# Kernel tuning notes

Hardware: AMD Instinct MI355X
Metric: run time of the kernel (lower is better)

Reference implementation:

```python
import jax, jax.numpy as jnp
import numpy as np

D_MODEL = 256
NHEAD = 8
HEAD_DIM = D_MODEL // NHEAD
CLIP = 10.0


def setup_inputs() -> dict:
    key = jax.random.key(0)
    k1, k2, k3, k4 = jax.random.split(key, 4)
    B, N = 4, 256
    nodes = jax.random.normal(k1, (B, N, D_MODEL), dtype=jnp.float32)
    edges = jax.random.normal(k2, (B, N, N, D_MODEL), dtype=jnp.float32)
    # torch nn.Linear default init: U(-1/sqrt(in), 1/sqrt(in))
    bound = 1.0 / np.sqrt(D_MODEL)
    W = jax.random.uniform(k3, (D_MODEL, D_MODEL), minval=-bound, maxval=bound, dtype=jnp.float32)
    b = jax.random.uniform(k4, (D_MODEL,), minval=-bound, maxval=bound, dtype=jnp.float32)
    return {"nodes": nodes, "edges": edges, "W": W, "b": b}


def reference(nodes, edges, W, b):
    B, N, _ = nodes.shape
    H, Dh = NHEAD, HEAD_DIM

    def proj(x):  # torch Linear: x @ W.T + b
        return x @ W.T + b

    # Node projections: the module applies the SAME linear to q, k, v
    node_p = proj(nodes).reshape(B, N, H, Dh)
    nq, nk, nv = node_p, node_p, node_p
    # Edge projections (same linear for q and k)
    edge_p = proj(edges).reshape(B, N, N, H, Dh)
    eq, ek = edge_p, edge_p

    query = eq + nq[:, :, None, :, :]   # (B,N,N,H,Dh)
    key = ek + nk[:, None, :, :, :]     # (B,N,N,H,Dh)
    scores = jnp.einsum('bijhd,bijhd->bhij', query, key) / np.sqrt(Dh).astype(np.float32)
    scores = CLIP * jnp.tanh(scores)
    attn = jax.nn.softmax(scores, axis=-1)  # (B,H,N,N)
    # output = attn @ values (values transposed to (B,H,N,Dh))
    out = jnp.einsum('bhij,bjhd->bihd', attn, nv).reshape(B, N, D_MODEL)
    out = proj(out)
    return (out, attn)
```

## Files before the change

### kernel.cpp

```cpp
#include <hip/hip_runtime.h>
#include <hip/hip_bf16.h>
#include <math.h>

typedef short short8 __attribute__((ext_vector_type(8)));
typedef float f32x4 __attribute__((ext_vector_type(4)));

__device__ __forceinline__ unsigned short f2bf(float x) {
    unsigned u = __float_as_uint(x);
    u += 0x7FFF + ((u >> 16) & 1);
    return (unsigned short)(u >> 16);
}
__device__ __forceinline__ float bf2f(unsigned short h) {
    return __uint_as_float(((unsigned)h) << 16);
}

__device__ __forceinline__ void cvt2(float f0, float f1,
                                     unsigned short& h0, unsigned short& h1,
                                     unsigned short& l0, unsigned short& l1) {
    __hip_bfloat162 h = __float22bfloat162_rn(float2{f0, f1});
    unsigned hu = *(unsigned*)&h;
    h0 = (unsigned short)(hu & 0xFFFFu);
    h1 = (unsigned short)(hu >> 16);
    float r0 = f0 - __uint_as_float((hu & 0xFFFFu) << 16);
    float r1 = f1 - __uint_as_float(hu & 0xFFFF0000u);
    __hip_bfloat162 lo = __float22bfloat162_rn(float2{r0, r1});
    unsigned lu = *(unsigned*)&lo;
    l0 = (unsigned short)(lu & 0xFFFFu);
    l1 = (unsigned short)(lu >> 16);
}

__device__ __forceinline__ float tanh10(float y) {
    float e = __expf(2.f * y);
    return 10.f * (e - 1.f) / (e + 1.f);
}

#define GLDS16(gp, lp)                                                        \
    __builtin_amdgcn_global_load_lds(                                         \
        (const __attribute__((address_space(1))) void*)(gp),                  \
        (__attribute__((address_space(3))) void*)(lp), 16, 0, 0)

__global__ __launch_bounds__(256) void k_prep(const float* __restrict__ W,
                                              float* __restrict__ Wt,
                                              unsigned short* __restrict__ Whi,
                                              unsigned short* __restrict__ Wlo) {
    int d = blockIdx.x, k = threadIdx.x;
    float w = W[d * 256 + k];
    Wt[k * 256 + d] = w;
    unsigned short hi = f2bf(w);
    Whi[d * 256 + k] = hi;
    Wlo[d * 256 + k] = f2bf(w - bf2f(hi));
}

__global__ __launch_bounds__(256) void k_node_proj(const float* __restrict__ nodes,
                                                   const float* __restrict__ Wt,
                                                   const float* __restrict__ bias,
                                                   float* __restrict__ np_) {
    int row = blockIdx.x;
    int d = threadIdx.x;
    __shared__ float xl[256];
    xl[d] = nodes[row * 256 + d];
    __syncthreads();
    float a[8] = {0.f, 0.f, 0.f, 0.f, 0.f, 0.f, 0.f, 0.f};
#pragma unroll 4
    for (int k = 0; k < 256; k += 8) {
#pragma unroll
        for (int q = 0; q < 8; ++q)
            a[q] = fmaf(xl[k + q], Wt[(k + q) * 256 + d], a[q]);
    }
    np_[row * 256 + d] =
        bias[d] + ((a[0] + a[1]) + (a[2] + a[3])) + ((a[4] + a[5]) + (a[6] + a[7]));
}

__global__ __launch_bounds__(256) void k_edge_mfma(const float* __restrict__ edges,
                                                   const unsigned short* __restrict__ Whi,
                                                   const unsigned short* __restrict__ Wlo,
                                                   const float* __restrict__ bias,
                                                   const float* __restrict__ np_,
                                                   float* __restrict__ attn) {
    __shared__ unsigned short Eh[128 * 32], El[128 * 32];
    __shared__ unsigned short Wh[128 * 32], Wl[128 * 32];
    __shared__ float npi[128];
    __shared__ float sc[4][128];

    const int t = threadIdx.x;
    const int w = t >> 6, l = t & 63;
    const int tile = blockIdx.x >> 1;
    const int half = blockIdx.x & 1;
    const int m0 = tile * 128;
    const int bb = m0 >> 16;
    const int ii = (m0 >> 8) & 255;
    const int j0 = m0 & 255;
    const int n0 = half * 128;

    if (t < 32)
        ((float4*)npi)[t] = ((const float4*)(np_ + (size_t)(bb * 256 + ii) * 256 + n0))[t];

    f32x4 acc[4][4];
#pragma unroll
    for (int mt = 0; mt < 4; ++mt)
#pragma unroll
        for (int nt = 0; nt < 4; ++nt) acc[mt][nt] = (f32x4){0.f, 0.f, 0.f, 0.f};

    const int er = t >> 1, ehk = t & 1;
    const float* esrc = edges + (size_t)(m0 + er) * 256 + ehk * 16;

    const int wrow = (l >> 2), wq = l & 3;

    const int col = l & 15, g = l >> 4;
    const int wm = (w & 1) * 64, wn = (w >> 1) * 64;

    float4 ecur[4], enext[4];
#pragma unroll
    for (int q = 0; q < 4; ++q) ecur[q] = *(const float4*)(esrc + q * 4);

    for (int kc = 0; kc < 8; ++kc) {
#pragma unroll
        for (int s = 0; s < 2; ++s) {
            int base = w * 32 + s * 16;
            const unsigned short* gh =
                Whi + (size_t)(n0 + base + wrow) * 256 + kc * 32 + wq * 8;
            const unsigned short* gl =
                Wlo + (size_t)(n0 + base + wrow) * 256 + kc * 32 + wq * 8;
            GLDS16(gh, Wh + base * 32);
            GLDS16(gl, Wl + base * 32);
        }
        {
            unsigned short hi[16], lo[16];
#pragma unroll
            for (int q = 0; q < 4; ++q) {
                cvt2(ecur[q].x, ecur[q].y, hi[q * 4 + 0], hi[q * 4 + 1],
                     lo[q * 4 + 0], lo[q * 4 + 1]);
                cvt2(ecur[q].z, ecur[q].w, hi[q * 4 + 2], hi[q * 4 + 3],
                     lo[q * 4 + 2], lo[q * 4 + 3]);
            }
            *(short8*)(Eh + er * 32 + ehk * 16)     = *(short8*)&hi[0];
            *(short8*)(Eh + er * 32 + ehk * 16 + 8) = *(short8*)&hi[8];
            *(short8*)(El + er * 32 + ehk * 16)     = *(short8*)&lo[0];
            *(short8*)(El + er * 32 + ehk * 16 + 8) = *(short8*)&lo[8];
        }
        if (kc < 7) {
#pragma unroll
            for (int q = 0; q < 4; ++q)
                enext[q] = *(const float4*)(esrc + (kc + 1) * 32 + q * 4);
        }
        __syncthreads();
        short8 Ah[4], Al[4];
#pragma unroll
        for (int mt = 0; mt < 4; ++mt) {
            Ah[mt] = *(const short8*)(Eh + (wm + mt * 16 + col) * 32 + g * 8);
            Al[mt] = *(const short8*)(El + (wm + mt * 16 + col) * 32 + g * 8);
        }
#pragma unroll
        for (int nt = 0; nt < 4; ++nt) {
            short8 Bh = *(const short8*)(Wh + (wn + nt * 16 + col) * 32 + g * 8);
            short8 Bl = *(const short8*)(Wl + (wn + nt * 16 + col) * 32 + g * 8);
#pragma unroll
            for (int mt = 0; mt < 4; ++mt) {
                acc[mt][nt] = __builtin_amdgcn_mfma_f32_16x16x32_bf16(Ah[mt], Bh, acc[mt][nt], 0, 0, 0);
                acc[mt][nt] = __builtin_amdgcn_mfma_f32_16x16x32_bf16(Ah[mt], Bl, acc[mt][nt], 0, 0, 0);
                acc[mt][nt] = __builtin_amdgcn_mfma_f32_16x16x32_bf16(Al[mt], Bh, acc[mt][nt], 0, 0, 0);
            }
        }
        __syncthreads();
#pragma unroll
        for (int q = 0; q < 4; ++q) ecur[q] = enext[q];
    }

    const float isq = 0.17677669529663687f;
    float bv[4], nv[4];
#pragma unroll
    for (int nt = 0; nt < 4; ++nt) {
        int dl = wn + nt * 16 + col;
        bv[nt] = bias[n0 + dl];
        nv[nt] = npi[dl];
    }
    const int hl0 = (w >> 1) * 2;
#pragma unroll
    for (int mt = 0; mt < 4; ++mt) {
#pragma unroll
        for (int r = 0; r < 4; ++r) {
            int el = wm + mt * 16 + g * 4 + r;
            int j = j0 + el;
            const float* npj = np_ + (size_t)(bb * 256 + j) * 256 + n0 + wn;
            float p0 = acc[mt][0][r] + bv[0];
            float p1 = acc[mt][1][r] + bv[1];
            float p2 = acc[mt][2][r] + bv[2];
            float p3 = acc[mt][3][r] + bv[3];
            float s0 = (p0 + nv[0]) * (p0 + npj[col]) +
                       (p1 + nv[1]) * (p1 + npj[16 + col]);
            float s1 = (p2 + nv[2]) * (p2 + npj[32 + col]) +
                       (p3 + nv[3]) * (p3 + npj[48 + col]);
#pragma unroll
            for (int m = 1; m < 16; m <<= 1) {
                s0 += __shfl_xor(s0, m, 64);
                s1 += __shfl_xor(s1, m, 64);
            }
            if (col == 0) {
                sc[hl0][el]     = tanh10(s0 * isq);
                sc[hl0 + 1][el] = tanh10(s1 * isq);
            }
        }
    }
    __syncthreads();
    if (t < 128) {
        int hl = t >> 5, q = t & 31;
        float4 v = *(float4*)&sc[hl][q * 4];
        *(float4*)(attn + (((size_t)(bb * 8 + half * 4 + hl) * 256 + ii) << 8) + j0 + q * 4) = v;
    }
}

__global__ __launch_bounds__(256) void k_softmax(float* __restrict__ attn) {
    int row = (blockIdx.x * 256 + threadIdx.x) >> 6;
    int lane = threadIdx.x & 63;
    float4* rowp = (float4*)(attn + (size_t)row * 256);
    float4 v = rowp[lane];
    float m = fmaxf(fmaxf(v.x, v.y), fmaxf(v.z, v.w));
#pragma unroll
    for (int s = 1; s < 64; s <<= 1) m = fmaxf(m, __shfl_xor(m, s, 64));
    v.x = __expf(v.x - m); v.y = __expf(v.y - m);
    v.z = __expf(v.z - m); v.w = __expf(v.w - m);
    float sum = v.x + v.y + v.z + v.w;
#pragma unroll
    for (int s = 1; s < 64; s <<= 1) sum += __shfl_xor(sum, s, 64);
    float inv = 1.f / sum;
    v.x *= inv; v.y *= inv; v.z *= inv; v.w *= inv;
    rowp[lane] = v;
}

__global__ __launch_bounds__(256) void k_out(const float* __restrict__ attn,
                                             const float* __restrict__ np_,
                                             const float* __restrict__ Wt,
                                             const float* __restrict__ bias,
                                             float* __restrict__ out) {
    int bi = blockIdx.x;
    int bb = bi >> 8, ii = bi & 255;
    int d = threadIdx.x;
    __shared__ float at[8 * 256];
    __shared__ float xl[256];
#pragma unroll
    for (int s = 0; s < 2; ++s) {
        int idx = d + s * 256;
        int h = idx >> 6, q = idx & 63;
        ((float4*)at)[idx] =
            ((const float4*)(attn + ((size_t)(bb * 8 + h) * 256 + ii) * 256))[q];
    }
    __syncthreads();
    int h = d >> 5;
    const float* npb = np_ + (size_t)bb * 65536 + d;
    const float* ath = at + h * 256;
    float a[8] = {0.f, 0.f, 0.f, 0.f, 0.f, 0.f, 0.f, 0.f};
#pragma unroll 2
    for (int j = 0; j < 256; j += 8) {
#pragma unroll
        for (int q = 0; q < 8; ++q)
            a[q] = fmaf(ath[j + q], npb[(size_t)(j + q) * 256], a[q]);
    }
    xl[d] = ((a[0] + a[1]) + (a[2] + a[3])) + ((a[4] + a[5]) + (a[6] + a[7]));
    __syncthreads();
    float c[8] = {bias[d], 0.f, 0.f, 0.f, 0.f, 0.f, 0.f, 0.f};
#pragma unroll 2
    for (int k = 0; k < 256; k += 8) {
#pragma unroll
        for (int q = 0; q < 8; ++q)
            c[q] = fmaf(xl[k + q], Wt[(k + q) * 256 + d], c[q]);
    }
    out[bi * 256 + d] =
        ((c[0] + c[1]) + (c[2] + c[3])) + ((c[4] + c[5]) + (c[6] + c[7]));
}

extern "C" void kernel_launch(void* const* d_in, const int* in_sizes, int n_in,
                              void* d_out, int out_size, void* d_ws, size_t ws_size,
                              hipStream_t stream) {
    (void)in_sizes; (void)n_in; (void)out_size; (void)ws_size;
    const float* nodes = (const float*)d_in[0];
    const float* edges = (const float*)d_in[1];
    const float* W     = (const float*)d_in[2];
    const float* bias  = (const float*)d_in[3];

    float* out  = (float*)d_out;
    float* attn = out + 262144;

    float* np_ = (float*)d_ws;
    float* Wt  = np_ + 262144;
    unsigned short* Whi = (unsigned short*)(Wt + 65536);
    unsigned short* Wlo = Whi + 65536;

    hipLaunchKernelGGL(k_prep,      dim3(256),  dim3(256), 0, stream, W, Wt, Whi, Wlo);
    hipLaunchKernelGGL(k_node_proj, dim3(1024), dim3(256), 0, stream, nodes, Wt, bias, np_);
    hipLaunchKernelGGL(k_edge_mfma, dim3(4096), dim3(256), 0, stream, edges, Whi, Wlo, bias, np_, attn);
    hipLaunchKernelGGL(k_softmax,   dim3(2048), dim3(256), 0, stream, attn);
    hipLaunchKernelGGL(k_out,       dim3(1024), dim3(256), 0, stream, attn, np_, Wt, bias, out);
}
```

Before: 530.0 us.

## Load edge A-fragments directly to registers, double-buffer swizzled W tiles in LDS

The edge GEMM kernel now has each wave own 32 edge rows across all 128 output columns. Each thread loads its MFMA A-fragment from global memory straight into registers and converts it to bf16 hi/lo there, so edge data is no longer staged through LDS. The W hi/lo tiles are double-buffered in LDS with an XOR swizzle, baked into the prep kernel's layout, to avoid bank conflicts, which cuts the per-iteration barriers from two to one. Block indices are also remapped so that neighbouring blocks work on different tiles. In exchange there are more accumulator registers per thread (2x8 instead of 4x4), and each wave re-reads all of W from LDS.

Result: faster. 512.9 us (-3.2%).

```diff
diff --git a/kernel.cpp b/kernel.cpp
--- a/kernel.cpp
+++ b/kernel.cpp
@@ -14,19 +14,23 @@
     return __uint_as_float(((unsigned)h) << 16);
 }
 
-__device__ __forceinline__ void cvt2(float f0, float f1,
-                                     unsigned short& h0, unsigned short& h1,
-                                     unsigned short& l0, unsigned short& l1) {
-    __hip_bfloat162 h = __float22bfloat162_rn(float2{f0, f1});
-    unsigned hu = *(unsigned*)&h;
-    h0 = (unsigned short)(hu & 0xFFFFu);
-    h1 = (unsigned short)(hu >> 16);
-    float r0 = f0 - __uint_as_float((hu & 0xFFFFu) << 16);
+__device__ __forceinline__ void cvtpair(float f0, float f1, unsigned& hw, unsigned& lw) {
+    __hip_bfloat162 h2 = __float22bfloat162_rn(float2{f0, f1});
+    unsigned hu = *(unsigned*)&h2;
+    float r0 = f0 - __uint_as_float(hu << 16);
     float r1 = f1 - __uint_as_float(hu & 0xFFFF0000u);
-    __hip_bfloat162 lo = __float22bfloat162_rn(float2{r0, r1});
-    unsigned lu = *(unsigned*)&lo;
-    l0 = (unsigned short)(lu & 0xFFFFu);
-    l1 = (unsigned short)(lu >> 16);
+    __hip_bfloat162 l2 = __float22bfloat162_rn(float2{r0, r1});
+    hw = hu;
+    lw = *(unsigned*)&l2;
+}
+
+__device__ __forceinline__ void cvt8(const float4 a, const float4 b, short8& hi, short8& lo) {
+    union { unsigned u[4]; short8 s; } H, L;
+    cvtpair(a.x, a.y, H.u[0], L.u[0]);
+    cvtpair(a.z, a.w, H.u[1], L.u[1]);
+    cvtpair(b.x, b.y, H.u[2], L.u[2]);
+    cvtpair(b.z, b.w, H.u[3], L.u[3]);
+    hi = H.s; lo = L.s;
 }
 
 __device__ __forceinline__ float tanh10(float y) {
@@ -47,8 +51,11 @@
     float w = W[d * 256 + k];
     Wt[k * 256 + d] = w;
     unsigned short hi = f2bf(w);
-    Whi[d * 256 + k] = hi;
-    Wlo[d * 256 + k] = f2bf(w - bf2f(hi));
+    int s  = (k >> 3) & 3;
+    int sp = s ^ ((d >> 1) & 3);
+    int idx = d * 256 + (k & ~31) + sp * 8 + (k & 7);
+    Whi[idx] = hi;
+    Wlo[idx] = f2bf(w - bf2f(hi));
 }
 
 __global__ __launch_bounds__(256) void k_node_proj(const float* __restrict__ nodes,
@@ -77,127 +84,126 @@
                                                    const float* __restrict__ bias,
                                                    const float* __restrict__ np_,
                                                    float* __restrict__ attn) {
-    __shared__ unsigned short Eh[128 * 32], El[128 * 32];
-    __shared__ unsigned short Wh[128 * 32], Wl[128 * 32];
+    __shared__ unsigned short Wbuf[2][2][128 * 32];
     __shared__ float npi[128];
     __shared__ float sc[4][128];
 
     const int t = threadIdx.x;
     const int w = t >> 6, l = t & 63;
-    const int tile = blockIdx.x >> 1;
-    const int half = blockIdx.x & 1;
+
+    const int L = (blockIdx.x & 7) * 512 + (blockIdx.x >> 3);
+    const int tile = L >> 1, half = L & 1;
     const int m0 = tile * 128;
     const int bb = m0 >> 16;
     const int ii = (m0 >> 8) & 255;
     const int j0 = m0 & 255;
     const int n0 = half * 128;
 
+    const int col = l & 15, g = l >> 4;
+    const int wrow = l >> 2, wq = l & 3;
+
     if (t < 32)
         ((float4*)npi)[t] = ((const float4*)(np_ + (size_t)(bb * 256 + ii) * 256 + n0))[t];
 
-    f32x4 acc[4][4];
-#pragma unroll
-    for (int mt = 0; mt < 4; ++mt)
-#pragma unroll
-        for (int nt = 0; nt < 4; ++nt) acc[mt][nt] = (f32x4){0.f, 0.f, 0.f, 0.f};
-
-    const int er = t >> 1, ehk = t & 1;
-    const float* esrc = edges + (size_t)(m0 + er) * 256 + ehk * 16;
-
-    const int wrow = (l >> 2), wq = l & 3;
-
-    const int col = l & 15, g = l >> 4;
-    const int wm = (w & 1) * 64, wn = (w >> 1) * 64;
-
-    float4 ecur[4], enext[4];
-#pragma unroll
-    for (int q = 0; q < 4; ++q) ecur[q] = *(const float4*)(esrc + q * 4);
-
+    f32x4 acc[2][8];
+#pragma unroll
+    for (int mt = 0; mt < 2; ++mt)
+#pragma unroll
+        for (int nt = 0; nt < 8; ++nt) acc[mt][nt] = (f32x4){0.f, 0.f, 0.f, 0.f};
+
+    const float* ea0 = edges + (size_t)(m0 + w * 32 + col) * 256 + g * 8;
+    const float* ea1 = ea0 + 16 * 256;
+
+    const size_t wg0 = (size_t)(n0 + w * 32 + wrow) * 256 + wq * 8;
+    const size_t wg1 = wg0 + 16 * 256;
+
+    float4 e0a = *(const float4*)(ea0);
+    float4 e0b = *(const float4*)(ea0 + 4);
+    float4 e1a = *(const float4*)(ea1);
+    float4 e1b = *(const float4*)(ea1 + 4);
+    GLDS16(Whi + wg0, &Wbuf[0][0][(w * 32) * 32]);
+    GLDS16(Wlo + wg0, &Wbuf[0][1][(w * 32) * 32]);
+    GLDS16(Whi + wg1, &Wbuf[0][0][(w * 32 + 16) * 32]);
+    GLDS16(Wlo + wg1, &Wbuf[0][1][(w * 32 + 16) * 32]);
+
+    short8 Ah[2], Al[2];
+    cvt8(e0a, e0b, Ah[0], Al[0]);
+    cvt8(e1a, e1b, Ah[1], Al[1]);
+    __syncthreads();
+
+    const int swb = (g ^ ((col >> 1) & 3)) << 3;
+
+#pragma unroll 2
     for (int kc = 0; kc < 8; ++kc) {
-#pragma unroll
-        for (int s = 0; s < 2; ++s) {
-            int base = w * 32 + s * 16;
-            const unsigned short* gh =
-                Whi + (size_t)(n0 + base + wrow) * 256 + kc * 32 + wq * 8;
-            const unsigned short* gl =
-                Wlo + (size_t)(n0 + base + wrow) * 256 + kc * 32 + wq * 8;
-            GLDS16(gh, Wh + base * 32);
-            GLDS16(gl, Wl + base * 32);
-        }
-        {
-            unsigned short hi[16], lo[16];
-#pragma unroll
-            for (int q = 0; q < 4; ++q) {
-                cvt2(ecur[q].x, ecur[q].y, hi[q * 4 + 0], hi[q * 4 + 1],
-                     lo[q * 4 + 0], lo[q * 4 + 1]);
-                cvt2(ecur[q].z, ecur[q].w, hi[q * 4 + 2], hi[q * 4 + 3],
-                     lo[q * 4 + 2], lo[q * 4 + 3]);
-            }
-            *(short8*)(Eh + er * 32 + ehk * 16)     = *(short8*)&hi[0];
-            *(short8*)(Eh + er * 32 + ehk * 16 + 8) = *(short8*)&hi[8];
-            *(short8*)(El + er * 32 + ehk * 16)     = *(short8*)&lo[0];
-            *(short8*)(El + er * 32 + ehk * 16 + 8) = *(short8*)&lo[8];
-        }
+        float4 p0a, p0b, p1a, p1b;
         if (kc < 7) {
-#pragma unroll
-            for (int q = 0; q < 4; ++q)
-                enext[q] = *(const float4*)(esrc + (kc + 1) * 32 + q * 4);
+            const int nb = (kc + 1) & 1;
+            const size_t kofs = (size_t)(kc + 1) * 32;
+            GLDS16(Whi + wg0 + kofs, &Wbuf[nb][0][(w * 32) * 32]);
+            GLDS16(Wlo + wg0 + kofs, &Wbuf[nb][1][(w * 32) * 32]);
+            GLDS16(Whi + wg1 + kofs, &Wbuf[nb][0][(w * 32 + 16) * 32]);
+            GLDS16(Wlo + wg1 + kofs, &Wbuf[nb][1][(w * 32 + 16) * 32]);
+            p0a = *(const float4*)(ea0 + (kc + 1) * 32);
+            p0b = *(const float4*)(ea0 + (kc + 1) * 32 + 4);
+            p1a = *(const float4*)(ea1 + (kc + 1) * 32);
+            p1b = *(const float4*)(ea1 + (kc + 1) * 32 + 4);
+        }
+        const unsigned short* bh = &Wbuf[kc & 1][0][0] + col * 32 + swb;
+        const unsigned short* bl = &Wbuf[kc & 1][1][0] + col * 32 + swb;
+#pragma unroll
+        for (int nt = 0; nt < 8; ++nt) {
+            short8 Bh = *(const short8*)(bh + nt * 512);
+            short8 Bl = *(const short8*)(bl + nt * 512);
+            acc[0][nt] = __builtin_amdgcn_mfma_f32_16x16x32_bf16(Ah[0], Bh, acc[0][nt], 0, 0, 0);
+            acc[1][nt] = __builtin_amdgcn_mfma_f32_16x16x32_bf16(Ah[1], Bh, acc[1][nt], 0, 0, 0);
+            acc[0][nt] = __builtin_amdgcn_mfma_f32_16x16x32_bf16(Ah[0], Bl, acc[0][nt], 0, 0, 0);
+            acc[1][nt] = __builtin_amdgcn_mfma_f32_16x16x32_bf16(Ah[1], Bl, acc[1][nt], 0, 0, 0);
+            acc[0][nt] = __builtin_amdgcn_mfma_f32_16x16x32_bf16(Al[0], Bh, acc[0][nt], 0, 0, 0);
+            acc[1][nt] = __builtin_amdgcn_mfma_f32_16x16x32_bf16(Al[1], Bh, acc[1][nt], 0, 0, 0);
+        }
+        if (kc < 7) {
+            cvt8(p0a, p0b, Ah[0], Al[0]);
+            cvt8(p1a, p1b, Ah[1], Al[1]);
         }
         __syncthreads();
-        short8 Ah[4], Al[4];
-#pragma unroll
-        for (int mt = 0; mt < 4; ++mt) {
-            Ah[mt] = *(const short8*)(Eh + (wm + mt * 16 + col) * 32 + g * 8);
-            Al[mt] = *(const short8*)(El + (wm + mt * 16 + col) * 32 + g * 8);
-        }
-#pragma unroll
-        for (int nt = 0; nt < 4; ++nt) {
-            short8 Bh = *(const short8*)(Wh + (wn + nt * 16 + col) * 32 + g * 8);
-            short8 Bl = *(const short8*)(Wl + (wn + nt * 16 + col) * 32 + g * 8);
-#pragma unroll
-            for (int mt = 0; mt < 4; ++mt) {
-                acc[mt][nt] = __builtin_amdgcn_mfma_f32_16x16x32_bf16(Ah[mt], Bh, acc[mt][nt], 0, 0, 0);
-                acc[mt][nt] = __builtin_amdgcn_mfma_f32_16x16x32_bf16(Ah[mt], Bl, acc[mt][nt], 0, 0, 0);
-                acc[mt][nt] = __builtin_amdgcn_mfma_f32_16x16x32_bf16(Al[mt], Bh, acc[mt][nt], 0, 0, 0);
-            }
-        }
-        __syncthreads();
-#pragma unroll
-        for (int q = 0; q < 4; ++q) ecur[q] = enext[q];
     }
 
     const float isq = 0.17677669529663687f;
-    float bv[4], nv[4];
-#pragma unroll
-    for (int nt = 0; nt < 4; ++nt) {
-        int dl = wn + nt * 16 + col;
+    float bv[8], nv[8];
+#pragma unroll
+    for (int nt = 0; nt < 8; ++nt) {
+        int dl = nt * 16 + col;
         bv[nt] = bias[n0 + dl];
         nv[nt] = npi[dl];
     }
-    const int hl0 = (w >> 1) * 2;
-#pragma unroll
-    for (int mt = 0; mt < 4; ++mt) {
+#pragma unroll
+    for (int mt = 0; mt < 2; ++mt) {
 #pragma unroll
         for (int r = 0; r < 4; ++r) {
-            int el = wm + mt * 16 + g * 4 + r;
+            int el = w * 32 + mt * 16 + g * 4 + r;
             int j = j0 + el;
-            const float* npj = np_ + (size_t)(bb * 256 + j) * 256 + n0 + wn;
-            float p0 = acc[mt][0][r] + bv[0];
-            float p1 = acc[mt][1][r] + bv[1];
-            float p2 = acc[mt][2][r] + bv[2];
-            float p3 = acc[mt][3][r] + bv[3];
-            float s0 = (p0 + nv[0]) * (p0 + npj[col]) +
-                       (p1 + nv[1]) * (p1 + npj[16 + col]);
-            float s1 = (p2 + nv[2]) * (p2 + npj[32 + col]) +
-                       (p3 + nv[3]) * (p3 + npj[48 + col]);
+            const float* npj = np_ + (size_t)(bb * 256 + j) * 256 + n0;
+            float p, s0 = 0.f, s1 = 0.f, s2 = 0.f, s3 = 0.f;
+            p = acc[mt][0][r] + bv[0]; s0 += (p + nv[0]) * (p + npj[col]);
+            p = acc[mt][1][r] + bv[1]; s0 += (p + nv[1]) * (p + npj[16 + col]);
+            p = acc[mt][2][r] + bv[2]; s1 += (p + nv[2]) * (p + npj[32 + col]);
+            p = acc[mt][3][r] + bv[3]; s1 += (p + nv[3]) * (p + npj[48 + col]);
+            p = acc[mt][4][r] + bv[4]; s2 += (p + nv[4]) * (p + npj[64 + col]);
+            p = acc[mt][5][r] + bv[5]; s2 += (p + nv[5]) * (p + npj[80 + col]);
+            p = acc[mt][6][r] + bv[6]; s3 += (p + nv[6]) * (p + npj[96 + col]);
+            p = acc[mt][7][r] + bv[7]; s3 += (p + nv[7]) * (p + npj[112 + col]);
 #pragma unroll
             for (int m = 1; m < 16; m <<= 1) {
                 s0 += __shfl_xor(s0, m, 64);
                 s1 += __shfl_xor(s1, m, 64);
+                s2 += __shfl_xor(s2, m, 64);
+                s3 += __shfl_xor(s3, m, 64);
             }
             if (col == 0) {
-                sc[hl0][el]     = tanh10(s0 * isq);
-                sc[hl0 + 1][el] = tanh10(s1 * isq);
+                sc[0][el] = tanh10(s0 * isq);
+                sc[1][el] = tanh10(s1 * isq);
+                sc[2][el] = tanh10(s2 * isq);
+                sc[3][el] = tanh10(s3 * isq);
             }
         }
     }
```
